# Kernel optimization log

Measured on AMD Instinct MI355X. Metric: run time of the kernel, lower is better.

The kernel has to match this reference:

```python
import jax, jax.numpy as jnp
import numpy as np

B, V, T, P, F, H = 256, 32, 48, 12, 4, 128


def setup_inputs() -> dict:
    key = jax.random.key(0)
    ks = jax.random.split(key, 12)
    s = 1.0 / np.sqrt(H)  # PyTorch LSTMCell/Linear init scale
    u = lambda k, shape: jax.random.uniform(k, shape, jnp.float32, -s, s)
    return {
        "sequence": jax.random.normal(ks[0], (B, V, T, F), jnp.float32),
        "dist_matrix": jax.random.uniform(ks[1], (B, V, V), jnp.float32),
        "bearing_matrix": jax.random.uniform(ks[2], (B, V, V), jnp.float32),
        "heading_matrix": jax.random.uniform(ks[3], (B, V, V), jnp.float32),
        "seq_mask": jnp.ones((B, V, T), jnp.float32),
        "op_mask": jnp.ones((B, V, P), jnp.float32),
        "W_ih": u(ks[4], (4 * H, F)),
        "W_hh": u(ks[5], (4 * H, H)),
        "b_ih": u(ks[6], (4 * H,)),
        "b_hh": u(ks[7], (4 * H,)),
        "W_out": u(ks[8], (F, H)),
        "b_out": u(ks[9], (F,)),
    }


def reference(sequence, dist_matrix, bearing_matrix, heading_matrix,
              seq_mask, op_mask, W_ih, W_hh, b_ih, b_hh, W_out, b_out):
    # dist/bearing/heading matrices and masks are unused in the original forward.
    Bb, Vv, Tt, Ff = sequence.shape
    Hh = W_hh.shape[1]
    N = Bb * Vv  # all vessels share the same LSTMCell -> batch them together

    def cell(h, c, x):
        gates = x @ W_ih.T + b_ih + h @ W_hh.T + b_hh  # [N, 4H]
        i, f, g, o = jnp.split(gates, 4, axis=-1)       # torch gate order i,f,g,o
        c = jax.nn.sigmoid(f) * c + jax.nn.sigmoid(i) * jnp.tanh(g)
        h = jax.nn.sigmoid(o) * jnp.tanh(c)
        return h, c

    # ---- encode observed sequence ----
    x_seq = sequence.transpose(2, 0, 1, 3).reshape(Tt, N, Ff)  # [T, N, F]

    def enc_step(carry, x_t):
        h, c = carry
        h, c = cell(h, c, x_t)
        return (h, c), None

    h0 = jnp.zeros((N, Hh), sequence.dtype)
    (h, c), _ = jax.lax.scan(enc_step, (h0, h0), x_seq)

    prev = sequence[:, :, -1, :].reshape(N, Ff)

    def dec_step(carry, _):
        h, c, prev = carry
        h, c = cell(h, c, prev)
        out = h @ W_out.T + b_out  # [N, F]
        return (h, c, out), out

    _, outs = jax.lax.scan(dec_step, (h, c, prev), None, length=P)  # [P, N, F]
    output = outs.reshape(P, Bb, Vv, Ff).transpose(1, 2, 0, 3)      # [B, V, P, F]
    return output
```

## Files before the change

kernel.cpp:

```cpp
#include <hip/hip_runtime.h>


typedef __attribute__((ext_vector_type(8))) short short8;
typedef __attribute__((ext_vector_type(4))) float floatx4;

static __device__ __forceinline__ short f2bf(float x) {
  union { float f; unsigned u; } v; v.f = x;
  unsigned r = (v.u + 0x7FFFu + ((v.u >> 16) & 1u)) >> 16;
  return (short)r;
}
static __device__ __forceinline__ float sigm(float x) {
  return __builtin_amdgcn_rcpf(1.0f + __expf(-x));
}
static __device__ __forceinline__ float tanh_(float x) {
  return 1.0f - 2.0f * __builtin_amdgcn_rcpf(1.0f + __expf(2.0f * x));
}

__global__ __launch_bounds__(512, 2) void lstm_fused(
    const float* __restrict__ seq,
    const float* __restrict__ W_ih, const float* __restrict__ W_hh,
    const float* __restrict__ b_ih, const float* __restrict__ b_hh,
    const float* __restrict__ W_out, const float* __restrict__ b_out,
    float* __restrict__ out)
{
  __shared__ __align__(16) short h_lds[2][32][136];
  __shared__ __align__(16) float x_buf[32][4];

  const int tid = threadIdx.x;
  const int w   = tid >> 6;
  const int L   = tid & 63;
  const int l15 = L & 15;
  const int l4  = L >> 4;
  const int base_row = blockIdx.x << 5;

  short8 frag1[4][4];
  short8 wout[4];
  float  wih[4][4];
  float  bias[4];
  float  c_st[2][4];
  float  bo;

  {
    short* hp = &h_lds[0][0][0];
    for (int i = tid; i < 32 * 136; i += 512) hp[i] = 0;
  }

  #pragma unroll
  for (int g = 0; g < 4; ++g) {
    const int col = g * 128 + w * 16 + l15;
    bias[g] = b_ih[col] + b_hh[col];
    #pragma unroll
    for (int f = 0; f < 4; ++f) wih[g][f] = W_ih[col * 4 + f];
    #pragma unroll
    for (int kk = 0; kk < 4; ++kk) {
      const float* src = W_hh + col * 128 + kk * 32 + l4 * 8;
      short8 fr;
      #pragma unroll
      for (int i = 0; i < 8; ++i) fr[i] = f2bf(src[i]);
      frag1[g][kk] = fr;
    }
  }
  bo = (l15 < 4) ? b_out[l15] : 0.0f;
  #pragma unroll
  for (int kk = 0; kk < 4; ++kk) {
    short8 fr;
    #pragma unroll
    for (int i = 0; i < 8; ++i)
      fr[i] = (l15 < 4) ? f2bf(W_out[l15 * 128 + kk * 32 + l4 * 8 + i]) : (short)0;
    wout[kk] = fr;
  }
  #pragma unroll
  for (int rg = 0; rg < 2; ++rg)
    #pragma unroll
    for (int r = 0; r < 4; ++r) c_st[rg][r] = 0.0f;

  __syncthreads();

  int cur = 0;

  for (int t = 0; t < 48; ++t) {
    #pragma unroll
    for (int rg = 0; rg < 2; ++rg) {
      short8 afr[4];
      #pragma unroll
      for (int kk = 0; kk < 4; ++kk)
        afr[kk] = *(const short8*)&h_lds[cur][rg * 16 + l15][kk * 32 + l4 * 8];

      floatx4 acc[4];
      #pragma unroll
      for (int g = 0; g < 4; ++g) acc[g] = (floatx4){bias[g], bias[g], bias[g], bias[g]};

      #pragma unroll
      for (int r = 0; r < 4; ++r) {
        const int row = base_row + rg * 16 + l4 * 4 + r;
        const floatx4 x4 = *(const floatx4*)(seq + row * 192 + t * 4);
        #pragma unroll
        for (int g = 0; g < 4; ++g) {
          float s = acc[g][r];
          #pragma unroll
          for (int f = 0; f < 4; ++f) s = fmaf(x4[f], wih[g][f], s);
          acc[g][r] = s;
        }
      }

      #pragma unroll
      for (int g = 0; g < 4; ++g)
        #pragma unroll
        for (int kk = 0; kk < 4; ++kk)
          acc[g] = __builtin_amdgcn_mfma_f32_16x16x32_bf16(afr[kk], frag1[g][kk], acc[g], 0, 0, 0);

      #pragma unroll
      for (int r = 0; r < 4; ++r) {
        const float ig = sigm(acc[0][r]);
        const float fg = sigm(acc[1][r]);
        const float gg = tanh_(acc[2][r]);
        const float og = sigm(acc[3][r]);
        const float c  = fg * c_st[rg][r] + ig * gg;
        c_st[rg][r] = c;
        const float h = og * tanh_(c);
        h_lds[cur ^ 1][rg * 16 + l4 * 4 + r][w * 16 + l15] = f2bf(h);
      }
    }
    __syncthreads();
    cur ^= 1;
  }

  for (int p = 0; p < 12; ++p) {
    #pragma unroll
    for (int rg = 0; rg < 2; ++rg) {
      short8 afr[4];
      #pragma unroll
      for (int kk = 0; kk < 4; ++kk)
        afr[kk] = *(const short8*)&h_lds[cur][rg * 16 + l15][kk * 32 + l4 * 8];

      floatx4 acc[4];
      #pragma unroll
      for (int g = 0; g < 4; ++g) acc[g] = (floatx4){bias[g], bias[g], bias[g], bias[g]};

      #pragma unroll
      for (int r = 0; r < 4; ++r) {
        const int rloc = rg * 16 + l4 * 4 + r;
        floatx4 x4;
        if (p == 0) x4 = *(const floatx4*)(seq + (base_row + rloc) * 192 + 47 * 4);
        else        x4 = *(const floatx4*)&x_buf[rloc][0];
        #pragma unroll
        for (int g = 0; g < 4; ++g) {
          float s = acc[g][r];
          #pragma unroll
          for (int f = 0; f < 4; ++f) s = fmaf(x4[f], wih[g][f], s);
          acc[g][r] = s;
        }
      }

      #pragma unroll
      for (int g = 0; g < 4; ++g)
        #pragma unroll
        for (int kk = 0; kk < 4; ++kk)
          acc[g] = __builtin_amdgcn_mfma_f32_16x16x32_bf16(afr[kk], frag1[g][kk], acc[g], 0, 0, 0);

      #pragma unroll
      for (int r = 0; r < 4; ++r) {
        const float ig = sigm(acc[0][r]);
        const float fg = sigm(acc[1][r]);
        const float gg = tanh_(acc[2][r]);
        const float og = sigm(acc[3][r]);
        const float c  = fg * c_st[rg][r] + ig * gg;
        c_st[rg][r] = c;
        const float h = og * tanh_(c);
        h_lds[cur ^ 1][rg * 16 + l4 * 4 + r][w * 16 + l15] = f2bf(h);
      }
    }
    __syncthreads();

    if (w == 0) {
      #pragma unroll
      for (int rg = 0; rg < 2; ++rg) {
        short8 afr[4];
        #pragma unroll
        for (int kk = 0; kk < 4; ++kk)
          afr[kk] = *(const short8*)&h_lds[cur ^ 1][rg * 16 + l15][kk * 32 + l4 * 8];
        floatx4 acco = (floatx4){bo, bo, bo, bo};
        #pragma unroll
        for (int kk = 0; kk < 4; ++kk)
          acco = __builtin_amdgcn_mfma_f32_16x16x32_bf16(afr[kk], wout[kk], acco, 0, 0, 0);
        if (l15 < 4) {
          #pragma unroll
          for (int r = 0; r < 4; ++r) {
            const int rloc = rg * 16 + l4 * 4 + r;
            out[(base_row + rloc) * 48 + p * 4 + l15] = acco[r];
            x_buf[rloc][l15] = acco[r];
          }
        }
      }
    }
    __syncthreads();
    cur ^= 1;
  }
}

extern "C" void kernel_launch(void* const* d_in, const int* in_sizes, int n_in,
                              void* d_out, int out_size, void* d_ws, size_t ws_size,
                              hipStream_t stream) {
  const float* seq   = (const float*)d_in[0];
  const float* W_ih  = (const float*)d_in[6];
  const float* W_hh  = (const float*)d_in[7];
  const float* b_ih  = (const float*)d_in[8];
  const float* b_hh  = (const float*)d_in[9];
  const float* W_out = (const float*)d_in[10];
  const float* b_out = (const float*)d_in[11];
  lstm_fused<<<256, 512, 0, stream>>>(seq, W_ih, W_hh, b_ih, b_hh, W_out, b_out,
                                      (float*)d_out);
}
```

Before: 219.3 us.

## Fold output projection into decoder recurrence and halve rows per block

The decoder's feedback input prev = h@W_out^T + b_out is folded algebraically into the recurrent weights (W_hh + W_ih·W_out) and bias (b + W_ih·b_out) after the first decode step. This removes the per-step output-projection dependency and the second barrier from the recurrence's critical path. Output computation rotates across waves and no longer feeds the next step. Each block now handles 16 rows instead of 32 with twice as many blocks and higher launch-bound occupancy, trading per-block work for more parallelism. The fused weights are rounded to bf16 again, which adds a little numerical error.

```diff
diff --git a/kernel.cpp b/kernel.cpp
--- a/kernel.cpp
+++ b/kernel.cpp
@@ -9,6 +9,10 @@
   unsigned r = (v.u + 0x7FFFu + ((v.u >> 16) & 1u)) >> 16;
   return (short)r;
 }
+static __device__ __forceinline__ float bf2f(short b) {
+  union { unsigned u; float f; } v; v.u = ((unsigned)(unsigned short)b) << 16;
+  return v.f;
+}
 static __device__ __forceinline__ float sigm(float x) {
   return __builtin_amdgcn_rcpf(1.0f + __expf(-x));
 }
@@ -16,41 +20,48 @@
   return 1.0f - 2.0f * __builtin_amdgcn_rcpf(1.0f + __expf(2.0f * x));
 }
 
-__global__ __launch_bounds__(512, 2) void lstm_fused(
+__global__ __launch_bounds__(512, 4) void lstm_fused(
     const float* __restrict__ seq,
     const float* __restrict__ W_ih, const float* __restrict__ W_hh,
     const float* __restrict__ b_ih, const float* __restrict__ b_hh,
     const float* __restrict__ W_out, const float* __restrict__ b_out,
     float* __restrict__ out)
 {
-  __shared__ __align__(16) short h_lds[2][32][136];
-  __shared__ __align__(16) float x_buf[32][4];
+  __shared__ __align__(16) short h_lds[2][16][136];
+  __shared__ __align__(16) float wout_f32[4][128];
 
   const int tid = threadIdx.x;
   const int w   = tid >> 6;
   const int L   = tid & 63;
   const int l15 = L & 15;
   const int l4  = L >> 4;
-  const int base_row = blockIdx.x << 5;
+  const int base_row = blockIdx.x << 4;
 
   short8 frag1[4][4];
   short8 wout[4];
   float  wih[4][4];
   float  bias[4];
-  float  c_st[2][4];
+  float  bias_dec[4];
+  float  c_st[4];
   float  bo;
 
   {
     short* hp = &h_lds[0][0][0];
-    for (int i = tid; i < 32 * 136; i += 512) hp[i] = 0;
+    for (int i = tid; i < 16 * 136; i += 512) hp[i] = 0;
+    wout_f32[tid >> 7][tid & 127] = W_out[tid];
   }
 
   #pragma unroll
   for (int g = 0; g < 4; ++g) {
     const int col = g * 128 + w * 16 + l15;
     bias[g] = b_ih[col] + b_hh[col];
-    #pragma unroll
-    for (int f = 0; f < 4; ++f) wih[g][f] = W_ih[col * 4 + f];
+    float bd = bias[g];
+    #pragma unroll
+    for (int f = 0; f < 4; ++f) {
+      wih[g][f] = W_ih[col * 4 + f];
+      bd = fmaf(b_out[f], wih[g][f], bd);
+    }
+    bias_dec[g] = bd;
     #pragma unroll
     for (int kk = 0; kk < 4; ++kk) {
       const float* src = W_hh + col * 128 + kk * 32 + l4 * 8;
@@ -70,30 +81,70 @@
     wout[kk] = fr;
   }
   #pragma unroll
-  for (int rg = 0; rg < 2; ++rg)
-    #pragma unroll
-    for (int r = 0; r < 4; ++r) c_st[rg][r] = 0.0f;
+  for (int r = 0; r < 4; ++r) c_st[r] = 0.0f;
 
   __syncthreads();
 
   int cur = 0;
 
   for (int t = 0; t < 48; ++t) {
-    #pragma unroll
-    for (int rg = 0; rg < 2; ++rg) {
-      short8 afr[4];
-      #pragma unroll
-      for (int kk = 0; kk < 4; ++kk)
-        afr[kk] = *(const short8*)&h_lds[cur][rg * 16 + l15][kk * 32 + l4 * 8];
-
-      floatx4 acc[4];
+    short8 afr[4];
+    #pragma unroll
+    for (int kk = 0; kk < 4; ++kk)
+      afr[kk] = *(const short8*)&h_lds[cur][l15][kk * 32 + l4 * 8];
+
+    floatx4 acc[4];
+    #pragma unroll
+    for (int g = 0; g < 4; ++g) acc[g] = (floatx4){bias[g], bias[g], bias[g], bias[g]};
+
+    #pragma unroll
+    for (int r = 0; r < 4; ++r) {
+      const int row = base_row + l4 * 4 + r;
+      const floatx4 x4 = *(const floatx4*)(seq + row * 192 + t * 4);
+      #pragma unroll
+      for (int g = 0; g < 4; ++g) {
+        float s = acc[g][r];
+        #pragma unroll
+        for (int f = 0; f < 4; ++f) s = fmaf(x4[f], wih[g][f], s);
+        acc[g][r] = s;
+      }
+    }
+
+    #pragma unroll
+    for (int g = 0; g < 4; ++g)
+      #pragma unroll
+      for (int kk = 0; kk < 4; ++kk)
+        acc[g] = __builtin_amdgcn_mfma_f32_16x16x32_bf16(afr[kk], frag1[g][kk], acc[g], 0, 0, 0);
+
+    #pragma unroll
+    for (int r = 0; r < 4; ++r) {
+      const float ig = sigm(acc[0][r]);
+      const float fg = sigm(acc[1][r]);
+      const float gg = tanh_(acc[2][r]);
+      const float og = sigm(acc[3][r]);
+      const float c  = fg * c_st[r] + ig * gg;
+      c_st[r] = c;
+      const float h = og * tanh_(c);
+      h_lds[cur ^ 1][l4 * 4 + r][w * 16 + l15] = f2bf(h);
+    }
+    __syncthreads();
+    cur ^= 1;
+  }
+
+  for (int p = 0; p < 12; ++p) {
+    short8 afr[4];
+    #pragma unroll
+    for (int kk = 0; kk < 4; ++kk)
+      afr[kk] = *(const short8*)&h_lds[cur][l15][kk * 32 + l4 * 8];
+
+    floatx4 acc[4];
+    if (p == 0) {
       #pragma unroll
       for (int g = 0; g < 4; ++g) acc[g] = (floatx4){bias[g], bias[g], bias[g], bias[g]};
-
       #pragma unroll
       for (int r = 0; r < 4; ++r) {
-        const int row = base_row + rg * 16 + l4 * 4 + r;
-        const floatx4 x4 = *(const floatx4*)(seq + row * 192 + t * 4);
+        const int row = base_row + l4 * 4 + r;
+        const floatx4 x4 = *(const floatx4*)(seq + row * 192 + 47 * 4);
         #pragma unroll
         for (int g = 0; g < 4; ++g) {
           float s = acc[g][r];
@@ -102,98 +153,65 @@
           acc[g][r] = s;
         }
       }
-
+    } else {
       #pragma unroll
       for (int g = 0; g < 4; ++g)
-        #pragma unroll
-        for (int kk = 0; kk < 4; ++kk)
-          acc[g] = __builtin_amdgcn_mfma_f32_16x16x32_bf16(afr[kk], frag1[g][kk], acc[g], 0, 0, 0);
-
-      #pragma unroll
-      for (int r = 0; r < 4; ++r) {
-        const float ig = sigm(acc[0][r]);
-        const float fg = sigm(acc[1][r]);
-        const float gg = tanh_(acc[2][r]);
-        const float og = sigm(acc[3][r]);
-        const float c  = fg * c_st[rg][r] + ig * gg;
-        c_st[rg][r] = c;
-        const float h = og * tanh_(c);
-        h_lds[cur ^ 1][rg * 16 + l4 * 4 + r][w * 16 + l15] = f2bf(h);
+        acc[g] = (floatx4){bias_dec[g], bias_dec[g], bias_dec[g], bias_dec[g]};
+    }
+
+    #pragma unroll
+    for (int g = 0; g < 4; ++g)
+      #pragma unroll
+      for (int kk = 0; kk < 4; ++kk)
+        acc[g] = __builtin_amdgcn_mfma_f32_16x16x32_bf16(afr[kk], frag1[g][kk], acc[g], 0, 0, 0);
+
+    #pragma unroll
+    for (int r = 0; r < 4; ++r) {
+      const float ig = sigm(acc[0][r]);
+      const float fg = sigm(acc[1][r]);
+      const float gg = tanh_(acc[2][r]);
+      const float og = sigm(acc[3][r]);
+      const float c  = fg * c_st[r] + ig * gg;
+      c_st[r] = c;
+      const float h = og * tanh_(c);
+      h_lds[cur ^ 1][l4 * 4 + r][w * 16 + l15] = f2bf(h);
+    }
+    __syncthreads();
+
+    if (w == (p & 7)) {
+      short8 ofr[4];
+      #pragma unroll
+      for (int kk = 0; kk < 4; ++kk)
+        ofr[kk] = *(const short8*)&h_lds[cur ^ 1][l15][kk * 32 + l4 * 8];
+      floatx4 acco = (floatx4){bo, bo, bo, bo};
+      #pragma unroll
+      for (int kk = 0; kk < 4; ++kk)
+        acco = __builtin_amdgcn_mfma_f32_16x16x32_bf16(ofr[kk], wout[kk], acco, 0, 0, 0);
+      if (l15 < 4) {
+        #pragma unroll
+        for (int r = 0; r < 4; ++r)
+          out[(base_row + l4 * 4 + r) * 48 + p * 4 + l15] = acco[r];
       }
     }
-    __syncthreads();
-    cur ^= 1;
-  }
-
-  for (int p = 0; p < 12; ++p) {
-    #pragma unroll
-    for (int rg = 0; rg < 2; ++rg) {
-      short8 afr[4];
-      #pragma unroll
-      for (int kk = 0; kk < 4; ++kk)
-        afr[kk] = *(const short8*)&h_lds[cur][rg * 16 + l15][kk * 32 + l4 * 8];
-
-      floatx4 acc[4];
-      #pragma unroll
-      for (int g = 0; g < 4; ++g) acc[g] = (floatx4){bias[g], bias[g], bias[g], bias[g]};
-
-      #pragma unroll
-      for (int r = 0; r < 4; ++r) {
-        const int rloc = rg * 16 + l4 * 4 + r;
-        floatx4 x4;
-        if (p == 0) x4 = *(const floatx4*)(seq + (base_row + rloc) * 192 + 47 * 4);
-        else        x4 = *(const floatx4*)&x_buf[rloc][0];
-        #pragma unroll
-        for (int g = 0; g < 4; ++g) {
-          float s = acc[g][r];
+
+    if (p == 0) {
+      #pragma unroll
+      for (int g = 0; g < 4; ++g)
+        #pragma unroll
+        for (int kk = 0; kk < 4; ++kk) {
+          short8 fr = frag1[g][kk];
           #pragma unroll
-          for (int f = 0; f < 4; ++f) s = fmaf(x4[f], wih[g][f], s);
-          acc[g][r] = s;
+          for (int i = 0; i < 8; ++i) {
+            const int k = kk * 32 + l4 * 8 + i;
+            float v = bf2f(fr[i]);
+            #pragma unroll
+            for (int f = 0; f < 4; ++f) v = fmaf(wih[g][f], wout_f32[f][k], v);
+            fr[i] = f2bf(v);
+          }
+          frag1[g][kk] = fr;
         }
-      }
-
-      #pragma unroll
-      for (int g = 0; g < 4; ++g)
-        #pragma unroll
-        for (int kk = 0; kk < 4; ++kk)
-          acc[g] = __builtin_amdgcn_mfma_f32_16x16x32_bf16(afr[kk], frag1[g][kk], acc[g], 0, 0, 0);
-
-      #pragma unroll
-      for (int r = 0; r < 4; ++r) {
-        const float ig = sigm(acc[0][r]);
-        const float fg = sigm(acc[1][r]);
-        const float gg = tanh_(acc[2][r]);
-        const float og = sigm(acc[3][r]);
-        const float c  = fg * c_st[rg][r] + ig * gg;
-        c_st[rg][r] = c;
-        const float h = og * tanh_(c);
-        h_lds[cur ^ 1][rg * 16 + l4 * 4 + r][w * 16 + l15] = f2bf(h);
-      }
-    }
-    __syncthreads();
-
-    if (w == 0) {
-      #pragma unroll
-      for (int rg = 0; rg < 2; ++rg) {
-        short8 afr[4];
-        #pragma unroll
-        for (int kk = 0; kk < 4; ++kk)
-          afr[kk] = *(const short8*)&h_lds[cur ^ 1][rg * 16 + l15][kk * 32 + l4 * 8];
-        floatx4 acco = (floatx4){bo, bo, bo, bo};
-        #pragma unroll
-        for (int kk = 0; kk < 4; ++kk)
-          acco = __builtin_amdgcn_mfma_f32_16x16x32_bf16(afr[kk], wout[kk], acco, 0, 0, 0);
-        if (l15 < 4) {
-          #pragma unroll
-          for (int r = 0; r < 4; ++r) {
-            const int rloc = rg * 16 + l4 * 4 + r;
-            out[(base_row + rloc) * 48 + p * 4 + l15] = acco[r];
-            x_buf[rloc][l15] = acco[r];
-          }
-        }
-      }
-    }
-    __syncthreads();
+    }
+
     cur ^= 1;
   }
 }
@@ -208,6 +226,6 @@
   const float* b_hh  = (const float*)d_in[9];
   const float* W_out = (const float*)d_in[10];
   const float* b_out = (const float*)d_in[11];
-  lstm_fused<<<256, 512, 0, stream>>>(seq, W_ih, W_hh, b_ih, b_hh, W_out, b_out,
+  lstm_fused<<<512, 512, 0, stream>>>(seq, W_ih, W_hh, b_ih, b_hh, W_out, b_out,
                                       (float*)d_out);
 }
```

New measurement: 688.2 us. 214% more time.
